# Performance work log

Measured on AMD Instinct MI355X. Metric: run time of the kernel, lower is better.

Reference implementation:

```python
import jax, jax.numpy as jnp
import numpy as np

TAU = 1.0   # ltc_params['tau_constant']
DT = 0.1    # LTCCell default dt
UNFOLDS = 6 # ltc_params['ode_unfolds']
B, S, D, H, O = 512, 512, 128, 128, 1


def setup_inputs() -> dict:
    key = jax.random.key(0)
    ks = jax.random.split(key, 7)
    sc = lambda n: 1.0 / np.sqrt(n)
    return {
        "x":    jax.random.normal(ks[0], (B, S, D), dtype=jnp.float32),
        "W_in": jax.random.normal(ks[1], (H, D), dtype=jnp.float32) * sc(D),
        "b_in": jax.random.normal(ks[2], (H,), dtype=jnp.float32) * sc(D),
        "W_r":  jax.random.normal(ks[3], (H, H), dtype=jnp.float32) * sc(H),
        "b_r":  jax.random.normal(ks[4], (H,), dtype=jnp.float32) * sc(H),
        "W_fc": jax.random.normal(ks[5], (O, H), dtype=jnp.float32) * sc(H),
        "b_fc": jax.random.normal(ks[6], (O,), dtype=jnp.float32) * sc(H),
    }


def reference(x, W_in, b_in, W_r, b_r, W_fc, b_fc):
    # input_map(x[:, t]) is invariant across the inner unfold loop -> precompute once.
    xin_all = jnp.einsum('bsd,hd->bsh', x, W_in) + b_in  # [B,S,H]

    def step(h, xin):  # h: [B,H], xin: [B,H]
        for _ in range(UNFOLDS):  # small fixed count, unrolled
            v = jnp.tanh(xin + h @ W_r.T + b_r)
            h = h + DT * (-h / TAU + v)
        return h, None

    h0 = jnp.zeros((x.shape[0], W_r.shape[0]), dtype=x.dtype)
    h, _ = jax.lax.scan(step, h0, jnp.swapaxes(xin_all, 0, 1))  # scan over seq
    return (h @ W_fc.T + b_fc).squeeze(-1)  # [B]
```

## Files before the change

### kernel.cpp

```cpp
#include <hip/hip_runtime.h>


typedef _Float16 v2h __attribute__((ext_vector_type(2)));

#define S_LEN 512
#define HDIM 128
#define NUNF 6
#define DTC 0.1f

__device__ __forceinline__ float fast_tanh(float y) {
    float u = __expf(2.0f * y);
    return 1.0f - __fdividef(2.0f, u + 1.0f);
}

__global__ __launch_bounds__(256, 2)
void ltc_kernel(const float* __restrict__ x,
                const float* __restrict__ W_in,
                const float* __restrict__ b_in,
                const float* __restrict__ W_r,
                const float* __restrict__ b_r,
                const float* __restrict__ W_fc,
                const float* __restrict__ b_fc,
                float* __restrict__ out)
{
    const int b     = blockIdx.x;
    const int tid   = threadIdx.x;
    const int o     = tid >> 1;
    const int kh    = tid & 1;
    const int kbase = kh * 64;

    __shared__ __align__(16) _Float16 hbuf[2][HDIM];
    __shared__ __align__(16) _Float16 xbuf[2][HDIM];
    __shared__ float red[4];

    v2h wr[32], wi[32];
    {
        const float4* wrp = reinterpret_cast<const float4*>(W_r  + o * HDIM + kbase);
        const float4* wip = reinterpret_cast<const float4*>(W_in + o * HDIM + kbase);
#pragma unroll
        for (int j = 0; j < 16; ++j) {
            float4 f = wrp[j];
            wr[2*j]   = v2h{(_Float16)f.x, (_Float16)f.y};
            wr[2*j+1] = v2h{(_Float16)f.z, (_Float16)f.w};
            float4 g = wip[j];
            wi[2*j]   = v2h{(_Float16)g.x, (_Float16)g.y};
            wi[2*j+1] = v2h{(_Float16)g.z, (_Float16)g.w};
        }
    }
    const float binv = b_in[o];
    const float brv  = b_r[o];

    const float* x_row = x + (size_t)b * S_LEN * HDIM;

    float h_o = 0.0f;

    if (tid < HDIM) {
        xbuf[0][tid] = (_Float16)x_row[tid];
        hbuf[0][tid] = (_Float16)0.0f;
    }
    __syncthreads();

    for (int s = 0; s < S_LEN; ++s) {
        float xnext = 0.0f;
        if (tid < HDIM && s + 1 < S_LEN)
            xnext = x_row[(size_t)(s + 1) * HDIM + tid];

        float xin_o;
        {
            const float4* hp = reinterpret_cast<const float4*>(&xbuf[s & 1][kbase]);
            float4 hv[8];
#pragma unroll
            for (int j = 0; j < 8; ++j) hv[j] = hp[j];
            const v2h* hh = reinterpret_cast<const v2h*>(hv);
            float a0 = 0.f, a1 = 0.f, a2 = 0.f, a3 = 0.f;
#pragma unroll
            for (int j = 0; j < 32; j += 4) {
                a0 = __builtin_amdgcn_fdot2(wi[j],   hh[j],   a0, false);
                a1 = __builtin_amdgcn_fdot2(wi[j+1], hh[j+1], a1, false);
                a2 = __builtin_amdgcn_fdot2(wi[j+2], hh[j+2], a2, false);
                a3 = __builtin_amdgcn_fdot2(wi[j+3], hh[j+3], a3, false);
            }
            float sum = (a0 + a1) + (a2 + a3);
            sum += __shfl_xor(sum, 1);
            xin_o = sum + binv;
        }

#pragma unroll
        for (int u = 0; u < NUNF; ++u) {
            const float4* hp = reinterpret_cast<const float4*>(&hbuf[u & 1][kbase]);
            float4 hv[8];
#pragma unroll
            for (int j = 0; j < 8; ++j) hv[j] = hp[j];
            const v2h* hh = reinterpret_cast<const v2h*>(hv);
            float a0 = 0.f, a1 = 0.f, a2 = 0.f, a3 = 0.f;
#pragma unroll
            for (int j = 0; j < 32; j += 4) {
                a0 = __builtin_amdgcn_fdot2(wr[j],   hh[j],   a0, false);
                a1 = __builtin_amdgcn_fdot2(wr[j+1], hh[j+1], a1, false);
                a2 = __builtin_amdgcn_fdot2(wr[j+2], hh[j+2], a2, false);
                a3 = __builtin_amdgcn_fdot2(wr[j+3], hh[j+3], a3, false);
            }
            float sum = (a0 + a1) + (a2 + a3);
            sum += __shfl_xor(sum, 1);
            float yv = xin_o + brv + sum;
            float v  = fast_tanh(yv);
            h_o = h_o + DTC * (v - h_o);
            if ((tid & 1) == 0)
                hbuf[(u + 1) & 1][o] = (_Float16)h_o;
            if (u == NUNF - 1 && tid < HDIM && s + 1 < S_LEN)
                xbuf[(s + 1) & 1][tid] = (_Float16)xnext;
            __syncthreads();
        }
    }

    float partial = 0.0f;
    if ((tid & 1) == 0) partial = h_o * W_fc[o];
#pragma unroll
    for (int d = 1; d < 64; d <<= 1) partial += __shfl_xor(partial, d);
    if ((tid & 63) == 0) red[tid >> 6] = partial;
    __syncthreads();
    if (tid == 0) out[b] = red[0] + red[1] + red[2] + red[3] + b_fc[0];
}

extern "C" void kernel_launch(void* const* d_in, const int* in_sizes, int n_in,
                              void* d_out, int out_size, void* d_ws, size_t ws_size,
                              hipStream_t stream) {
    const float* x    = (const float*)d_in[0];
    const float* W_in = (const float*)d_in[1];
    const float* b_in = (const float*)d_in[2];
    const float* W_r  = (const float*)d_in[3];
    const float* b_r  = (const float*)d_in[4];
    const float* W_fc = (const float*)d_in[5];
    const float* b_fc = (const float*)d_in[6];
    float* outp = (float*)d_out;
    (void)in_sizes; (void)n_in; (void)out_size; (void)d_ws; (void)ws_size;
    ltc_kernel<<<dim3(512), dim3(256), 0, stream>>>(x, W_in, b_in, W_r, b_r, W_fc, b_fc, outp);
}
```

Measured before the change: 1.537 ms.

## Use single-wavefront blocks with two outputs per lane to eliminate barriers

Each batch row is now processed by one 64-lane wavefront, with each lane computing two hidden outputs over the full 128-wide reduction and holding both rows of W_r and W_in in registers. This removes all block-level barriers, the pairwise shuffle reduction, and the cross-wave final reduction. In exchange it quadruples per-lane dot-product work, raises register pressure substantially, and lowers the number of waves per CU available for latency hiding. It also relies on in-order LDS visibility within a single wave.

After: 3.150 ms. +104.9%, slower.

```diff
diff --git a/kernel.cpp b/kernel.cpp
--- a/kernel.cpp
+++ b/kernel.cpp
@@ -4,16 +4,39 @@
 typedef _Float16 v2h __attribute__((ext_vector_type(2)));
 
 #define S_LEN 512
-#define HDIM 128
-#define NUNF 6
-#define DTC 0.1f
+#define HDIM  128
+#define NUNF  6
+#define DTC   0.1f
 
 __device__ __forceinline__ float fast_tanh(float y) {
     float u = __expf(2.0f * y);
     return 1.0f - __fdividef(2.0f, u + 1.0f);
 }
 
-__global__ __launch_bounds__(256, 2)
+#define MATVEC128(WA, WB, BASE, R0, R1) do {                                   \
+    const float4* _hp = reinterpret_cast<const float4*>(BASE);                 \
+    float4 _hv[16];                                                            \
+    _Pragma("unroll")                                                          \
+    for (int _j = 0; _j < 16; ++_j) _hv[_j] = _hp[_j];                         \
+    const v2h* _hh = reinterpret_cast<const v2h*>(_hv);                        \
+    float _a0=0.f,_a1=0.f,_a2=0.f,_a3=0.f;                                     \
+    float _b0=0.f,_b1=0.f,_b2=0.f,_b3=0.f;                                     \
+    _Pragma("unroll")                                                          \
+    for (int _j = 0; _j < 64; _j += 4) {                                       \
+        _a0 = __builtin_amdgcn_fdot2(WA[_j],   _hh[_j],   _a0, false);         \
+        _a1 = __builtin_amdgcn_fdot2(WA[_j+1], _hh[_j+1], _a1, false);         \
+        _a2 = __builtin_amdgcn_fdot2(WA[_j+2], _hh[_j+2], _a2, false);         \
+        _a3 = __builtin_amdgcn_fdot2(WA[_j+3], _hh[_j+3], _a3, false);         \
+        _b0 = __builtin_amdgcn_fdot2(WB[_j],   _hh[_j],   _b0, false);         \
+        _b1 = __builtin_amdgcn_fdot2(WB[_j+1], _hh[_j+1], _b1, false);         \
+        _b2 = __builtin_amdgcn_fdot2(WB[_j+2], _hh[_j+2], _b2, false);         \
+        _b3 = __builtin_amdgcn_fdot2(WB[_j+3], _hh[_j+3], _b3, false);         \
+    }                                                                          \
+    R0 = (_a0 + _a1) + (_a2 + _a3);                                            \
+    R1 = (_b0 + _b1) + (_b2 + _b3);                                            \
+} while (0)
+
+__global__ __launch_bounds__(64, 1)
 void ltc_kernel(const float* __restrict__ x,
                 const float* __restrict__ W_in,
                 const float* __restrict__ b_in,
@@ -23,103 +46,81 @@
                 const float* __restrict__ b_fc,
                 float* __restrict__ out)
 {
-    const int b     = blockIdx.x;
-    const int tid   = threadIdx.x;
-    const int o     = tid >> 1;
-    const int kh    = tid & 1;
-    const int kbase = kh * 64;
+    const int b    = blockIdx.x;
+    const int lane = threadIdx.x;
+    const int o0   = lane << 1;
 
     __shared__ __align__(16) _Float16 hbuf[2][HDIM];
     __shared__ __align__(16) _Float16 xbuf[2][HDIM];
-    __shared__ float red[4];
 
-    v2h wr[32], wi[32];
+    v2h wr0[64], wr1[64], wi0[64], wi1[64];
     {
-        const float4* wrp = reinterpret_cast<const float4*>(W_r  + o * HDIM + kbase);
-        const float4* wip = reinterpret_cast<const float4*>(W_in + o * HDIM + kbase);
+        const float4* p0 = reinterpret_cast<const float4*>(W_r  + (size_t)o0 * HDIM);
+        const float4* p1 = reinterpret_cast<const float4*>(W_r  + (size_t)(o0 + 1) * HDIM);
+        const float4* q0 = reinterpret_cast<const float4*>(W_in + (size_t)o0 * HDIM);
+        const float4* q1 = reinterpret_cast<const float4*>(W_in + (size_t)(o0 + 1) * HDIM);
 #pragma unroll
-        for (int j = 0; j < 16; ++j) {
-            float4 f = wrp[j];
-            wr[2*j]   = v2h{(_Float16)f.x, (_Float16)f.y};
-            wr[2*j+1] = v2h{(_Float16)f.z, (_Float16)f.w};
-            float4 g = wip[j];
-            wi[2*j]   = v2h{(_Float16)g.x, (_Float16)g.y};
-            wi[2*j+1] = v2h{(_Float16)g.z, (_Float16)g.w};
+        for (int j = 0; j < 32; ++j) {
+            float4 f;
+            f = p0[j];
+            wr0[2*j]   = v2h{(_Float16)f.x, (_Float16)f.y};
+            wr0[2*j+1] = v2h{(_Float16)f.z, (_Float16)f.w};
+            f = p1[j];
+            wr1[2*j]   = v2h{(_Float16)f.x, (_Float16)f.y};
+            wr1[2*j+1] = v2h{(_Float16)f.z, (_Float16)f.w};
+            f = q0[j];
+            wi0[2*j]   = v2h{(_Float16)f.x, (_Float16)f.y};
+            wi0[2*j+1] = v2h{(_Float16)f.z, (_Float16)f.w};
+            f = q1[j];
+            wi1[2*j]   = v2h{(_Float16)f.x, (_Float16)f.y};
+            wi1[2*j+1] = v2h{(_Float16)f.z, (_Float16)f.w};
         }
     }
-    const float binv = b_in[o];
-    const float brv  = b_r[o];
+    const float2 biv = *reinterpret_cast<const float2*>(b_in + o0);
+    const float2 brv = *reinterpret_cast<const float2*>(b_r  + o0);
 
     const float* x_row = x + (size_t)b * S_LEN * HDIM;
 
-    float h_o = 0.0f;
+    {
+        float2 x0 = *reinterpret_cast<const float2*>(x_row + o0);
+        *reinterpret_cast<v2h*>(&xbuf[0][o0]) = v2h{(_Float16)x0.x, (_Float16)x0.y};
+        *reinterpret_cast<v2h*>(&hbuf[0][o0]) = v2h{(_Float16)0.f, (_Float16)0.f};
+    }
 
-    if (tid < HDIM) {
-        xbuf[0][tid] = (_Float16)x_row[tid];
-        hbuf[0][tid] = (_Float16)0.0f;
-    }
-    __syncthreads();
+    float h0 = 0.0f, h1 = 0.0f;
 
+#pragma unroll 1
     for (int s = 0; s < S_LEN; ++s) {
-        float xnext = 0.0f;
-        if (tid < HDIM && s + 1 < S_LEN)
-            xnext = x_row[(size_t)(s + 1) * HDIM + tid];
+        float2 xn = make_float2(0.0f, 0.0f);
+        if (s + 1 < S_LEN)
+            xn = *reinterpret_cast<const float2*>(x_row + (size_t)(s + 1) * HDIM + o0);
 
-        float xin_o;
-        {
-            const float4* hp = reinterpret_cast<const float4*>(&xbuf[s & 1][kbase]);
-            float4 hv[8];
-#pragma unroll
-            for (int j = 0; j < 8; ++j) hv[j] = hp[j];
-            const v2h* hh = reinterpret_cast<const v2h*>(hv);
-            float a0 = 0.f, a1 = 0.f, a2 = 0.f, a3 = 0.f;
-#pragma unroll
-            for (int j = 0; j < 32; j += 4) {
-                a0 = __builtin_amdgcn_fdot2(wi[j],   hh[j],   a0, false);
-                a1 = __builtin_amdgcn_fdot2(wi[j+1], hh[j+1], a1, false);
-                a2 = __builtin_amdgcn_fdot2(wi[j+2], hh[j+2], a2, false);
-                a3 = __builtin_amdgcn_fdot2(wi[j+3], hh[j+3], a3, false);
-            }
-            float sum = (a0 + a1) + (a2 + a3);
-            sum += __shfl_xor(sum, 1);
-            xin_o = sum + binv;
-        }
+        float xs0, xs1;
+        MATVEC128(wi0, wi1, &xbuf[s & 1][0], xs0, xs1);
+        const float xin0 = xs0 + biv.x;
+        const float xin1 = xs1 + biv.y;
 
 #pragma unroll
         for (int u = 0; u < NUNF; ++u) {
-            const float4* hp = reinterpret_cast<const float4*>(&hbuf[u & 1][kbase]);
-            float4 hv[8];
-#pragma unroll
-            for (int j = 0; j < 8; ++j) hv[j] = hp[j];
-            const v2h* hh = reinterpret_cast<const v2h*>(hv);
-            float a0 = 0.f, a1 = 0.f, a2 = 0.f, a3 = 0.f;
-#pragma unroll
-            for (int j = 0; j < 32; j += 4) {
-                a0 = __builtin_amdgcn_fdot2(wr[j],   hh[j],   a0, false);
-                a1 = __builtin_amdgcn_fdot2(wr[j+1], hh[j+1], a1, false);
-                a2 = __builtin_amdgcn_fdot2(wr[j+2], hh[j+2], a2, false);
-                a3 = __builtin_amdgcn_fdot2(wr[j+3], hh[j+3], a3, false);
-            }
-            float sum = (a0 + a1) + (a2 + a3);
-            sum += __shfl_xor(sum, 1);
-            float yv = xin_o + brv + sum;
-            float v  = fast_tanh(yv);
-            h_o = h_o + DTC * (v - h_o);
-            if ((tid & 1) == 0)
-                hbuf[(u + 1) & 1][o] = (_Float16)h_o;
-            if (u == NUNF - 1 && tid < HDIM && s + 1 < S_LEN)
-                xbuf[(s + 1) & 1][tid] = (_Float16)xnext;
-            __syncthreads();
+            float s0, s1;
+            MATVEC128(wr0, wr1, &hbuf[u & 1][0], s0, s1);
+            if (u == 0)
+                *reinterpret_cast<v2h*>(&xbuf[(s + 1) & 1][o0]) =
+                    v2h{(_Float16)xn.x, (_Float16)xn.y};
+            float v0 = fast_tanh(xin0 + brv.x + s0);
+            float v1 = fast_tanh(xin1 + brv.y + s1);
+            h0 += DTC * (v0 - h0);
+            h1 += DTC * (v1 - h1);
+            *reinterpret_cast<v2h*>(&hbuf[(u + 1) & 1][o0]) =
+                v2h{(_Float16)h0, (_Float16)h1};
         }
     }
 
-    float partial = 0.0f;
-    if ((tid & 1) == 0) partial = h_o * W_fc[o];
+    const float2 wfc = *reinterpret_cast<const float2*>(W_fc + o0);
+    float partial = h0 * wfc.x + h1 * wfc.y;
 #pragma unroll
     for (int d = 1; d < 64; d <<= 1) partial += __shfl_xor(partial, d);
-    if ((tid & 63) == 0) red[tid >> 6] = partial;
-    __syncthreads();
-    if (tid == 0) out[b] = red[0] + red[1] + red[2] + red[3] + b_fc[0];
+    if (lane == 0) out[b] = partial + b_fc[0];
 }
 
 extern "C" void kernel_launch(void* const* d_in, const int* in_sizes, int n_in,
@@ -134,5 +135,5 @@
     const float* b_fc = (const float*)d_in[6];
     float* outp = (float*)d_out;
     (void)in_sizes; (void)n_in; (void)out_size; (void)d_ws; (void)ws_size;
-    ltc_kernel<<<dim3(512), dim3(256), 0, stream>>>(x, W_in, b_in, W_r, b_r, W_fc, b_fc, outp);
+    ltc_kernel<<<dim3(512), dim3(64), 0, stream>>>(x, W_in, b_in, W_r, b_r, W_fc, b_fc, outp);
 }
```
